# Performance work log

Hardware: AMD Instinct MI355X
Metric: run time of the kernel (lower is better)

## Reference

```python
import jax, jax.numpy as jnp
import numpy as np

S, H, NH, DS = 4096, 1024, 2, 64   # seq_len, hidden, num_heads, static_in_size
HD = H // NH                        # head_dim = 512
EPS = 1e-5                          # eqx.nn.LayerNorm default eps


def setup_inputs() -> dict:
    key = jax.random.key(0)
    ks = jax.random.split(key, 11)
    sc = lambda n: 1.0 / np.sqrt(n)
    return {
        "inputs": jax.random.normal(ks[0], (S, H), jnp.float32),
        "static_data": jax.random.normal(ks[1], (DS,), jnp.float32),
        "base_mask": jax.random.randint(ks[2], (S,), 0, 2).astype(bool),
        "Wq": jax.random.normal(ks[3], (H, H), jnp.float32) * sc(H),
        "Wk": jax.random.normal(ks[4], (H, H), jnp.float32) * sc(H),
        "Wv": jax.random.normal(ks[5], (H, H), jnp.float32) * sc(H),
        "Wo": jax.random.normal(ks[6], (H, H), jnp.float32) * sc(H),
        "Ws": jax.random.normal(ks[7], (H, DS), jnp.float32) * sc(DS),
        "bs": jax.random.normal(ks[8], (H,), jnp.float32) * 0.01,
        "ln_w": jnp.ones((H,), jnp.float32),
        "ln_b": jnp.zeros((H,), jnp.float32),
    }


def reference(inputs, static_data, base_mask, Wq, Wk, Wv, Wo, Ws, bs, ln_w, ln_b):
    # static embedding injected into keys/values
    semb = Ws @ static_data + bs                      # [H]
    kv_in = inputs + semb[None, :]                    # [S, H]

    # per-head projections (eqx Linear: y = W @ x, no bias in MHA projections)
    q = (inputs @ Wq.T).reshape(S, NH, HD)
    k = (kv_in @ Wk.T).reshape(S, NH, HD)
    v = (kv_in @ Wv.T).reshape(S, NH, HD)

    logits = jnp.einsum('qhd,khd->hqk', q, k) / np.sqrt(HD)  # [NH, S, S]

    # head 0: irregular mask (base_mask broadcast over queries); head 1: all-ones
    irregular = jnp.broadcast_to(base_mask[None, :], (S, S))
    mask = jnp.stack([irregular, jnp.ones((S, S), bool)], axis=0)  # [2, S, S]
    logits = jnp.where(mask, logits, jnp.finfo(logits.dtype).min)

    attn = jax.nn.softmax(logits, axis=-1)
    ctx = jnp.einsum('hqk,khd->qhd', attn, v).reshape(S, H)
    out = ctx @ Wo.T                                  # output projection

    # dropout_rate = 0 -> identity; residual + per-token LayerNorm
    res = out + inputs
    mu = res.mean(-1, keepdims=True)
    var = res.var(-1, keepdims=True)
    return (res - mu) / jnp.sqrt(var + EPS) * ln_w + ln_b
```

## Files before the change

### kernel.cpp

```cpp
#include <hip/hip_runtime.h>
#include <stdint.h>

#define S_LEN  4096
#define HID    1024
#define NHEAD  2
#define HDIM   512
#define KS_STRIDE 520
#define LN_EPS 1e-5f
#define PADK   4224
#define CH1    832

typedef __bf16 bf16x8 __attribute__((ext_vector_type(8)));
typedef float  f32x4  __attribute__((ext_vector_type(4)));

__device__ __forceinline__ float b2f(unsigned short u) {
    return __uint_as_float(((unsigned int)u) << 16);
}
__device__ __forceinline__ unsigned short f2b(float f) {
    unsigned int u = __float_as_uint(f);
    u += 0x7FFFu + ((u >> 16) & 1u);
    return (unsigned short)(u >> 16);
}

__device__ __forceinline__ void async_cp16(const void* g, void* l) {
    __builtin_amdgcn_global_load_lds(
        (const __attribute__((address_space(1))) unsigned int*)g,
        (__attribute__((address_space(3))) unsigned int*)l, 16, 0, 0);
}

__global__ void k_cvt4s(const float* __restrict__ i0, const float* __restrict__ i1,
                        const float* __restrict__ i2, const float* __restrict__ i3,
                        unsigned short* __restrict__ o0, unsigned short* __restrict__ o1,
                        unsigned short* __restrict__ o2, unsigned short* __restrict__ o3,
                        const float* __restrict__ Ws, const float* __restrict__ sd,
                        const float* __restrict__ bs, float* __restrict__ semb,
                        const int* __restrict__ msk, int* __restrict__ cidx,
                        int* __restrict__ nactp) {
    int z = blockIdx.y;
    if (z == 4) {
        int j = blockIdx.x * blockDim.x + threadIdx.x;
        if (j >= HID) return;
        float acc = bs[j];
        const float* row = Ws + j * 64;
        #pragma unroll
        for (int d = 0; d < 64; ++d) acc += row[d] * sd[d];
        semb[j] = acc;
        return;
    }
    if (z == 5) {
        if (blockIdx.x != 0) return;
        __shared__ int cnts[256];
        __shared__ int bases[256];
        __shared__ int nact_s;
        int t = threadIdx.x;
        int c = 0;
        #pragma unroll
        for (int i = 0; i < 16; ++i) c += (msk[t * 16 + i] != 0);
        cnts[t] = c;
        __syncthreads();
        if (t == 0) {
            int b = 0;
            for (int k = 0; k < 256; ++k) { bases[k] = b; b += cnts[k]; }
            nactp[0] = b;
            nact_s   = b;
        }
        __syncthreads();
        int b = bases[t];
        #pragma unroll
        for (int i = 0; i < 16; ++i)
            if (msk[t * 16 + i] != 0) cidx[b++] = t * 16 + i;
        for (int j = nact_s + t; j < PADK; j += 256) cidx[j] = 0;
        return;
    }
    const float* in = z == 0 ? i0 : z == 1 ? i1 : z == 2 ? i2 : i3;
    unsigned short* o = z == 0 ? o0 : z == 1 ? o1 : z == 2 ? o2 : o3;
    int i = (blockIdx.x * blockDim.x + threadIdx.x) * 8;
    float4 a = *(const float4*)(in + i);
    float4 b = *(const float4*)(in + i + 4);
    unsigned short r[8] = {f2b(a.x), f2b(a.y), f2b(a.z), f2b(a.w),
                           f2b(b.x), f2b(b.y), f2b(b.z), f2b(b.w)};
    *(uint4*)(o + i) = *(const uint4*)r;
}

__global__ void k_kvin(const float* __restrict__ X,
                       const float* __restrict__ semb,
                       unsigned short* __restrict__ Xb,
                       unsigned short* __restrict__ kv) {
    int idx = (blockIdx.x * blockDim.x + threadIdx.x) * 8;
    if (idx >= S_LEN * HID) return;
    int col = idx & (HID - 1);
    float4 a = *(const float4*)(X + idx);
    float4 b = *(const float4*)(X + idx + 4);
    unsigned short xo[8] = {f2b(a.x), f2b(a.y), f2b(a.z), f2b(a.w),
                            f2b(b.x), f2b(b.y), f2b(b.z), f2b(b.w)};
    *(uint4*)(Xb + idx) = *(const uint4*)xo;
    unsigned short o[8];
    o[0] = f2b(a.x + semb[col + 0]);
    o[1] = f2b(a.y + semb[col + 1]);
    o[2] = f2b(a.z + semb[col + 2]);
    o[3] = f2b(a.w + semb[col + 3]);
    o[4] = f2b(b.x + semb[col + 4]);
    o[5] = f2b(b.y + semb[col + 5]);
    o[6] = f2b(b.z + semb[col + 6]);
    o[7] = f2b(b.w + semb[col + 7]);
    *(uint4*)(kv + idx) = *(const uint4*)o;
}

__device__ __forceinline__
void gemm128(const unsigned short* __restrict__ A,
             const unsigned short* __restrict__ B,
             unsigned short* __restrict__ Cb,
             int bx, int nx, int ldc,
             const int* __restrict__ ra, const int* __restrict__ rb) {
    __shared__ unsigned short As[2][128 * 32];
    __shared__ unsigned short Bs[2][128 * 32];
    int tid  = threadIdx.x;
    int wave = tid >> 6, lane = tid & 63;
    int quad = lane >> 4, l16 = lane & 15;
    int wm = wave >> 1, wn = wave & 1;
    int m0 = (bx / nx) * 128, n0 = (bx % nx) * 128;

    auto stage = [&](int k0, int b) {
        #pragma unroll
        for (int i = 0; i < 2; ++i) {
            int c = tid + i * 256;
            int arow = m0 + (c >> 2);
            if (ra) arow = ra[arow];
            int brow = n0 + (c >> 2);
            if (rb) brow = rb[brow];
            async_cp16(A + (size_t)arow * HID + k0 + (c & 3) * 8, As[b] + c * 8);
            async_cp16(B + (size_t)brow * HID + k0 + (c & 3) * 8, Bs[b] + c * 8);
        }
    };

    f32x4 zero = {0.f, 0.f, 0.f, 0.f};
    f32x4 acc[4][4];
    #pragma unroll
    for (int i = 0; i < 4; ++i)
        #pragma unroll
        for (int j = 0; j < 4; ++j) acc[i][j] = zero;

    stage(0, 0);
    for (int it = 0; it < HID / 32; ++it) {
        int b = it & 1;
        __syncthreads();
        if (it + 1 < HID / 32) stage((it + 1) * 32, b ^ 1);

        bf16x8 af[4], bfr[4];
        #pragma unroll
        for (int i = 0; i < 4; ++i)
            af[i] = *(const bf16x8*)(As[b] + (wm * 64 + i * 16 + l16) * 32 + quad * 8);
        #pragma unroll
        for (int j = 0; j < 4; ++j)
            bfr[j] = *(const bf16x8*)(Bs[b] + (wn * 64 + j * 16 + l16) * 32 + quad * 8);
        #pragma unroll
        for (int i = 0; i < 4; ++i)
            #pragma unroll
            for (int j = 0; j < 4; ++j)
                acc[i][j] = __builtin_amdgcn_mfma_f32_16x16x32_bf16(af[i], bfr[j], acc[i][j], 0, 0, 0);
    }

    #pragma unroll
    for (int i = 0; i < 4; ++i) {
        int rbase = m0 + wm * 64 + i * 16 + quad * 4;
        #pragma unroll
        for (int j = 0; j < 4; ++j) {
            int col = n0 + wn * 64 + j * 16 + l16;
            #pragma unroll
            for (int r = 0; r < 4; ++r)
                Cb[(size_t)(rbase + r) * ldc + col] = f2b(acc[i][j][r]);
        }
    }
}

__global__ __launch_bounds__(256)
void k_gemms(const unsigned short* __restrict__ Xb,
             const unsigned short* __restrict__ kvin,
             const unsigned short* __restrict__ Wqb,
             const unsigned short* __restrict__ Wkb,
             const unsigned short* __restrict__ Wvb,
             const int* __restrict__ cidx,
             unsigned short* __restrict__ Qb,
             unsigned short* __restrict__ Kb1,
             unsigned short* __restrict__ Vt1,
             unsigned short* __restrict__ Kc,
             unsigned short* __restrict__ Vtc) {
    int g = blockIdx.x;
    int b = (g & 7) * 97 + (g >> 3);
    if (b < 256)      gemm128(Xb,   Wqb,             Qb,  b,        8, HID,   nullptr, nullptr);
    else if (b < 384) gemm128(kvin, Wkb + 512 * HID, Kb1, b - 256,  4, 512,   nullptr, nullptr);
    else if (b < 512) gemm128(Wvb + 512 * HID, kvin, Vt1, b - 384, 32, S_LEN, nullptr, nullptr);
    else if (b < 644) gemm128(kvin, Wkb,             Kc,  b - 512,  4, 512,   cidx,    nullptr);
    else              gemm128(Wvb,  kvin,            Vtc, b - 644, 33, PADK,  nullptr, cidx);
}

__global__ __launch_bounds__(256)
void k_gemm_o(const unsigned short* __restrict__ Opart,
              const float* __restrict__ Lbuf,
              const unsigned short* __restrict__ B,
              float* __restrict__ Cf,
              const float* __restrict__ Xres) {
    __shared__ unsigned short As[2][64 * 32];
    __shared__ unsigned short Bs[2][128 * 32];
    const size_t SH2 = (size_t)S_LEN * 512;
    int tid  = threadIdx.x;
    int wave = tid >> 6, lane = tid & 63;
    int quad = lane >> 4, l16 = lane & 15;
    int bx = (blockIdx.x & 7) * 64 + (blockIdx.x >> 3);
    int m0 = (bx >> 3) * 64, n0 = (bx & 7) * 128;

    int arow  = m0 + (tid >> 2);
    int acol8 = (tid & 3) * 8;
    float rinv[NHEAD];
    {
        float l0 = Lbuf[arow] + Lbuf[S_LEN + arow] + Lbuf[2 * S_LEN + arow];
        float l1 = 0.f;
        #pragma unroll
        for (int z = 3; z < 8; ++z) l1 += Lbuf[z * S_LEN + arow];
        rinv[0] = 1.f / l0;
        rinv[1] = 1.f / l1;
    }

    auto stageB = [&](int k0, int b) {
        #pragma unroll
        for (int i = 0; i < 2; ++i) {
            int c = tid + i * 256;
            async_cp16(B + (n0 + (c >> 2)) * HID + k0 + (c & 3) * 8, Bs[b] + c * 8);
        }
    };
    auto stageA = [&](int k0, int b) {
        int h = k0 >> 9;
        float rv = rinv[h];
        int lk = (k0 & 511) + acol8;
        const unsigned short* ap = Opart + (h ? 3 * SH2 : 0) + (size_t)arow * 512 + lk;
        float s[8] = {0.f, 0.f, 0.f, 0.f, 0.f, 0.f, 0.f, 0.f};
        int nz = h ? 5 : 3;
        for (int z = 0; z < nz; ++z) {
            uint4 v = *(const uint4*)(ap + (size_t)z * SH2);
            unsigned short us[8];
            *(uint4*)us = v;
            #pragma unroll
            for (int e = 0; e < 8; ++e) s[e] += b2f(us[e]);
        }
        unsigned short o8[8];
        #pragma unroll
        for (int e = 0; e < 8; ++e) o8[e] = f2b(s[e] * rv);
        *(uint4*)(As[b] + tid * 8) = *(const uint4*)o8;
    };

    f32x4 zero = {0.f, 0.f, 0.f, 0.f};
    f32x4 acc[4][2];
    #pragma unroll
    for (int i = 0; i < 4; ++i)
        #pragma unroll
        for (int j = 0; j < 2; ++j) acc[i][j] = zero;

    stageB(0, 0);
    stageA(0, 0);
    for (int it = 0; it < HID / 32; ++it) {
        int b = it & 1;
        __syncthreads();
        if (it + 1 < HID / 32) {
            stageB((it + 1) * 32, b ^ 1);
            stageA((it + 1) * 32, b ^ 1);
        }
        bf16x8 af[4], bfr[2];
        #pragma unroll
        for (int i = 0; i < 4; ++i)
            af[i] = *(const bf16x8*)(As[b] + (i * 16 + l16) * 32 + quad * 8);
        #pragma unroll
        for (int j = 0; j < 2; ++j)
            bfr[j] = *(const bf16x8*)(Bs[b] + (wave * 32 + j * 16 + l16) * 32 + quad * 8);
        #pragma unroll
        for (int i = 0; i < 4; ++i)
            #pragma unroll
            for (int j = 0; j < 2; ++j)
                acc[i][j] = __builtin_amdgcn_mfma_f32_16x16x32_bf16(af[i], bfr[j], acc[i][j], 0, 0, 0);
    }

    #pragma unroll
    for (int i = 0; i < 4; ++i) {
        int rbase = m0 + i * 16 + quad * 4;
        #pragma unroll
        for (int j = 0; j < 2; ++j) {
            int col = n0 + wave * 32 + j * 16 + l16;
            #pragma unroll
            for (int r = 0; r < 4; ++r) {
                size_t o = (size_t)(rbase + r) * HID + col;
                Cf[o] = acc[i][j][r] + Xres[o];
            }
        }
    }
}

__global__ __launch_bounds__(512, 2)
void k_flash(const unsigned short* __restrict__ Q,
             const unsigned short* __restrict__ Kb1,
             const unsigned short* __restrict__ Vt1,
             const unsigned short* __restrict__ Kc,
             const unsigned short* __restrict__ Vtc,
             const int* __restrict__ nactp,
             unsigned short* __restrict__ Opart,
             float* __restrict__ Lbuf) {
    __shared__ unsigned short Ks[2][32 * KS_STRIDE];
    __shared__ __bf16 Ps[2][128][40];
    int tid  = threadIdx.x;
    int wave = tid >> 6, lane = tid & 63;
    int quad = lane >> 4, l16 = lane & 15;
    int x = blockIdx.x, qtile = blockIdx.y;
    int head  = (x >= 3) ? 1 : 0;
    int split = head ? x - 3 : x;
    int nact  = nactp[0];

    int nit, base, vrs;
    const unsigned short *Ksrc, *Vsrc;
    if (head == 0) {
        nit  = (nact + 95) / 96;
        base = split * nit * 32;
        Ksrc = Kc;  Vsrc = Vtc; vrs = PADK;
    } else {
        base = split * CH1;
        nit  = min(CH1 >> 5, (S_LEN - base) >> 5);
        Ksrc = Kb1; Vsrc = Vt1; vrs = S_LEN;
    }

    int qrow = qtile * 128 + wave * 16 + l16;
    const unsigned short* qp = Q + qrow * HID + head * HDIM;
    bf16x8 qf[16];
    #pragma unroll
    for (int t = 0; t < 16; ++t) qf[t] = *(const bf16x8*)(qp + t * 32 + quad * 8);

    float lsum[4];
    #pragma unroll
    for (int r = 0; r < 4; ++r) lsum[r] = 0.f;
    f32x4 zero = {0.f, 0.f, 0.f, 0.f};
    f32x4 oacc[8][4];
    #pragma unroll
    for (int mt = 0; mt < 8; ++mt)
        #pragma unroll
        for (int nt = 0; nt < 4; ++nt) oacc[mt][nt] = zero;

    const float scale = 0.044194173824159216f;
    const unsigned short* vptr = Vsrc + (size_t)(wave * 64 + l16) * vrs + base + quad * 8;

    auto stageK = [&](int kt, int buf) {
        int kb = base + kt * 32;
        #pragma unroll
        for (int i = 0; i < 4; ++i) {
            int c = tid + i * 512;
            int row = c >> 6, col = (c & 63) * 8;
            async_cp16(Ksrc + (size_t)(kb + row) * 512 + col, &Ks[buf][row * KS_STRIDE + col]);
        }
    };

    if (nit > 0) stageK(0, 0);

    bf16x8 vf[4];
    for (int it = 0; it < nit; ++it) {
        int cur = it & 1;
        __syncthreads();

        if (it + 1 < nit) stageK(it + 1, cur ^ 1);

        __builtin_amdgcn_s_setprio(1);
        if (it > 0) {
            #pragma unroll
            for (int mt = 0; mt < 8; ++mt) {
                bf16x8 pf = *(const bf16x8*)&Ps[cur ^ 1][mt * 16 + l16][quad * 8];
                #pragma unroll
                for (int nt = 0; nt < 4; ++nt)
                    oacc[mt][nt] = __builtin_amdgcn_mfma_f32_16x16x32_bf16(pf, vf[nt], oacc[mt][nt], 0, 0, 0);
            }
        }

        #pragma unroll
        for (int nt = 0; nt < 4; ++nt)
            vf[nt] = *(const bf16x8*)(vptr + (size_t)nt * 16 * vrs + it * 32);

        f32x4 sacc[2];
        sacc[0] = zero; sacc[1] = zero;
        #pragma unroll
        for (int nt = 0; nt < 2; ++nt)
            #pragma unroll
            for (int t = 0; t < 16; ++t) {
                bf16x8 kf = *(const bf16x8*)&Ks[cur][(nt * 16 + l16) * KS_STRIDE + t * 32 + quad * 8];
                sacc[nt] = __builtin_amdgcn_mfma_f32_16x16x32_bf16(qf[t], kf, sacc[nt], 0, 0, 0);
            }
        __builtin_amdgcn_s_setprio(0);

        bool keep0 = true, keep1 = true;
        if (head == 0) {
            int kb = base + it * 32;
            keep0 = kb + l16 < nact;
            keep1 = kb + 16 + l16 < nact;
        }
        #pragma unroll
        for (int r = 0; r < 4; ++r) {
            float p0 = keep0 ? __expf(fminf(sacc[0][r] * scale, 30.f)) : 0.f;
            float p1 = keep1 ? __expf(fminf(sacc[1][r] * scale, 30.f)) : 0.f;
            lsum[r] += p0 + p1;
            Ps[cur][wave * 16 + quad * 4 + r][l16]      = (__bf16)p0;
            Ps[cur][wave * 16 + quad * 4 + r][16 + l16] = (__bf16)p1;
        }
    }

    if (nit > 0) {
        int lastb = (nit - 1) & 1;
        __syncthreads();
        #pragma unroll
        for (int mt = 0; mt < 8; ++mt) {
            bf16x8 pf = *(const bf16x8*)&Ps[lastb][mt * 16 + l16][quad * 8];
            #pragma unroll
            for (int nt = 0; nt < 4; ++nt)
                oacc[mt][nt] = __builtin_amdgcn_mfma_f32_16x16x32_bf16(pf, vf[nt], oacc[mt][nt], 0, 0, 0);
        }
    }

    #pragma unroll
    for (int r = 0; r < 4; ++r) {
        float s = lsum[r];
        #pragma unroll
        for (int off = 1; off < 16; off <<= 1)
            s += __shfl_xor(s, off, 64);
        lsum[r] = s;
    }
    int slot = head ? 3 + split : split;
    int lrow = qtile * 128 + wave * 16 + quad * 4;
    if (l16 == 0) {
        #pragma unroll
        for (int r = 0; r < 4; ++r)
            Lbuf[slot * S_LEN + lrow + r] = lsum[r];
    }
    unsigned short* op = Opart + (size_t)slot * S_LEN * 512;
    #pragma unroll
    for (int mt = 0; mt < 8; ++mt)
        #pragma unroll
        for (int nt = 0; nt < 4; ++nt)
            #pragma unroll
            for (int r = 0; r < 4; ++r)
                op[(qtile * 128 + mt * 16 + quad * 4 + r) * 512 +
                   wave * 64 + nt * 16 + l16] = f2b(oacc[mt][nt][r]);
}

__global__ __launch_bounds__(256)
void k_ln(const float* __restrict__ res,
          const float* __restrict__ w,
          const float* __restrict__ b,
          float* __restrict__ out) {
    __shared__ float red[8];
    int s = blockIdx.x, tid = threadIdx.x;
    const float* row = res + s * HID;
    float x[4], s1 = 0.f, s2 = 0.f;
    #pragma unroll
    for (int i = 0; i < 4; ++i) {
        x[i] = row[tid + i * 256];
        s1 += x[i]; s2 += x[i] * x[i];
    }
    #pragma unroll
    for (int off = 1; off < 64; off <<= 1) {
        s1 += __shfl_xor(s1, off, 64);
        s2 += __shfl_xor(s2, off, 64);
    }
    int wave = tid >> 6;
    if ((tid & 63) == 0) { red[wave] = s1; red[4 + wave] = s2; }
    __syncthreads();
    s1 = red[0] + red[1] + red[2] + red[3];
    s2 = red[4] + red[5] + red[6] + red[7];
    float mu   = s1 * (1.f / HID);
    float var  = s2 * (1.f / HID) - mu * mu;
    float rstd = rsqrtf(var + LN_EPS);
    #pragma unroll
    for (int i = 0; i < 4; ++i) {
        int col = tid + i * 256;
        out[s * HID + col] = (x[i] - mu) * rstd * w[col] + b[col];
    }
}

extern "C" void kernel_launch(void* const* d_in, const int* in_sizes, int n_in,
                              void* d_out, int out_size, void* d_ws, size_t ws_size,
                              hipStream_t stream) {
    const float* X   = (const float*)d_in[0];
    const float* sd  = (const float*)d_in[1];
    const int*   msk = (const int*)d_in[2];
    const float* Wq  = (const float*)d_in[3];
    const float* Wk  = (const float*)d_in[4];
    const float* Wv  = (const float*)d_in[5];
    const float* Wo  = (const float*)d_in[6];
    const float* Wsp = (const float*)d_in[7];
    const float* bsp = (const float*)d_in[8];
    const float* lw  = (const float*)d_in[9];
    const float* lb  = (const float*)d_in[10];
    float* out = (float*)d_out;

    char* ws = (char*)d_ws;
    const size_t MB = 1ull << 20;
    float*          semb  = (float*)(ws);
    int*            cidx  = (int*)(ws + (16 << 10));
    int*            nactp = (int*)(ws + (48 << 10));
    float*          Lbuf  = (float*)(ws + (1ull << 16));
    unsigned short* Xb    = (unsigned short*)(ws + 1 * MB);
    unsigned short* kvin  = (unsigned short*)(ws + 9 * MB);
    unsigned short* Qb    = (unsigned short*)(ws + 17 * MB);
    unsigned short* Kb1   = (unsigned short*)(ws + 25 * MB);
    unsigned short* Vt1   = (unsigned short*)(ws + 29 * MB);
    unsigned short* Kc    = (unsigned short*)(ws + 33 * MB);
    unsigned short* Vtc   = (unsigned short*)(ws + 37 * MB + (256 << 10));
    unsigned short* Wqb   = (unsigned short*)(ws + 49 * MB);
    unsigned short* Wkb   = (unsigned short*)(ws + 51 * MB);
    unsigned short* Wvb   = (unsigned short*)(ws + 53 * MB);
    unsigned short* Wob   = (unsigned short*)(ws + 55 * MB);
    float*          resf  = (float*)(ws + 17 * MB);
    unsigned short* Opart = (unsigned short*)(ws + 57 * MB);

    const int SH = S_LEN * HID;
    const int WW = HID * HID;

    k_cvt4s<<<dim3(WW / 8 / 256, 6), dim3(256), 0, stream>>>(
        Wq, Wk, Wv, Wo, Wqb, Wkb, Wvb, Wob, Wsp, sd, bsp, semb, msk, cidx, nactp);

    k_kvin<<<dim3(SH / 8 / 256), dim3(256), 0, stream>>>(X, semb, Xb, kvin);

    k_gemms<<<dim3(776), dim3(256), 0, stream>>>(
        Xb, kvin, Wqb, Wkb, Wvb, cidx, Qb, Kb1, Vt1, Kc, Vtc);

    k_flash<<<dim3(8, S_LEN / 128), dim3(512), 0, stream>>>(
        Qb, Kb1, Vt1, Kc, Vtc, nactp, Opart, Lbuf);

    k_gemm_o<<<dim3(512), dim3(256), 0, stream>>>(Opart, Lbuf, Wob, resf, X);
    k_ln<<<dim3(S_LEN), dim3(256), 0, stream>>>(resf, lw, lb, out);
}
```

Before: 269.0 us.

## Fold static embedding into K/V GEMM bias, merge prep kernels, skip inactive tiles

```diff
diff --git a/kernel.cpp b/kernel.cpp
--- a/kernel.cpp
+++ b/kernel.cpp
@@ -35,11 +35,23 @@
                         const float* __restrict__ Ws, const float* __restrict__ sd,
                         const float* __restrict__ bs, float* __restrict__ semb,
                         const int* __restrict__ msk, int* __restrict__ cidx,
-                        int* __restrict__ nactp) {
-    int z = blockIdx.y;
-    if (z == 4) {
-        int j = blockIdx.x * blockDim.x + threadIdx.x;
-        if (j >= HID) return;
+                        int* __restrict__ nactp,
+                        const float* __restrict__ X, unsigned short* __restrict__ Xb) {
+    int b = blockIdx.x, tid = threadIdx.x;
+    if (b < 2048) {
+        int w = b >> 9, inner = b & 511;
+        const float* in = w == 0 ? i0 : w == 1 ? i1 : w == 2 ? i2 : i3;
+        unsigned short* o = w == 0 ? o0 : w == 1 ? o1 : w == 2 ? o2 : o3;
+        int i = (inner * 256 + tid) * 8;
+        float4 a = *(const float4*)(in + i);
+        float4 c = *(const float4*)(in + i + 4);
+        unsigned short r[8] = {f2b(a.x), f2b(a.y), f2b(a.z), f2b(a.w),
+                               f2b(c.x), f2b(c.y), f2b(c.z), f2b(c.w)};
+        *(uint4*)(o + i) = *(const uint4*)r;
+        return;
+    }
+    if (b < 2052) {
+        int j = (b - 2048) * 256 + tid;
         float acc = bs[j];
         const float* row = Ws + j * 64;
         #pragma unroll
@@ -47,63 +59,38 @@
         semb[j] = acc;
         return;
     }
-    if (z == 5) {
-        if (blockIdx.x != 0) return;
+    if (b == 2052) {
         __shared__ int cnts[256];
         __shared__ int bases[256];
         __shared__ int nact_s;
-        int t = threadIdx.x;
+        int t = tid;
         int c = 0;
         #pragma unroll
         for (int i = 0; i < 16; ++i) c += (msk[t * 16 + i] != 0);
         cnts[t] = c;
         __syncthreads();
         if (t == 0) {
-            int b = 0;
-            for (int k = 0; k < 256; ++k) { bases[k] = b; b += cnts[k]; }
-            nactp[0] = b;
-            nact_s   = b;
+            int bb = 0;
+            for (int k = 0; k < 256; ++k) { bases[k] = bb; bb += cnts[k]; }
+            nactp[0] = bb;
+            nact_s   = bb;
         }
         __syncthreads();
-        int b = bases[t];
+        int bb = bases[t];
         #pragma unroll
         for (int i = 0; i < 16; ++i)
-            if (msk[t * 16 + i] != 0) cidx[b++] = t * 16 + i;
+            if (msk[t * 16 + i] != 0) cidx[bb++] = t * 16 + i;
         for (int j = nact_s + t; j < PADK; j += 256) cidx[j] = 0;
         return;
     }
-    const float* in = z == 0 ? i0 : z == 1 ? i1 : z == 2 ? i2 : i3;
-    unsigned short* o = z == 0 ? o0 : z == 1 ? o1 : z == 2 ? o2 : o3;
-    int i = (blockIdx.x * blockDim.x + threadIdx.x) * 8;
-    float4 a = *(const float4*)(in + i);
-    float4 b = *(const float4*)(in + i + 4);
-    unsigned short r[8] = {f2b(a.x), f2b(a.y), f2b(a.z), f2b(a.w),
-                           f2b(b.x), f2b(b.y), f2b(b.z), f2b(b.w)};
-    *(uint4*)(o + i) = *(const uint4*)r;
-}
-
-__global__ void k_kvin(const float* __restrict__ X,
-                       const float* __restrict__ semb,
-                       unsigned short* __restrict__ Xb,
-                       unsigned short* __restrict__ kv) {
-    int idx = (blockIdx.x * blockDim.x + threadIdx.x) * 8;
-    if (idx >= S_LEN * HID) return;
-    int col = idx & (HID - 1);
-    float4 a = *(const float4*)(X + idx);
-    float4 b = *(const float4*)(X + idx + 4);
-    unsigned short xo[8] = {f2b(a.x), f2b(a.y), f2b(a.z), f2b(a.w),
-                            f2b(b.x), f2b(b.y), f2b(b.z), f2b(b.w)};
-    *(uint4*)(Xb + idx) = *(const uint4*)xo;
-    unsigned short o[8];
-    o[0] = f2b(a.x + semb[col + 0]);
-    o[1] = f2b(a.y + semb[col + 1]);
-    o[2] = f2b(a.z + semb[col + 2]);
-    o[3] = f2b(a.w + semb[col + 3]);
-    o[4] = f2b(b.x + semb[col + 4]);
-    o[5] = f2b(b.y + semb[col + 5]);
-    o[6] = f2b(b.z + semb[col + 6]);
-    o[7] = f2b(b.w + semb[col + 7]);
-    *(uint4*)(kv + idx) = *(const uint4*)o;
+    {
+        int idx = ((b - 2053) * 256 + tid) * 8;
+        float4 a = *(const float4*)(X + idx);
+        float4 c = *(const float4*)(X + idx + 4);
+        unsigned short r[8] = {f2b(a.x), f2b(a.y), f2b(a.z), f2b(a.w),
+                               f2b(c.x), f2b(c.y), f2b(c.z), f2b(c.w)};
+        *(uint4*)(Xb + idx) = *(const uint4*)r;
+    }
 }
 
 __device__ __forceinline__
@@ -111,14 +98,30 @@
              const unsigned short* __restrict__ B,
              unsigned short* __restrict__ Cb,
              int bx, int nx, int ldc,
-             const int* __restrict__ ra, const int* __restrict__ rb) {
+             const int* __restrict__ ra, const int* __restrict__ rb,
+             const float* __restrict__ semb, int bmode) {
     __shared__ unsigned short As[2][128 * 32];
     __shared__ unsigned short Bs[2][128 * 32];
+    __shared__ float pb[256];
     int tid  = threadIdx.x;
     int wave = tid >> 6, lane = tid & 63;
     int quad = lane >> 4, l16 = lane & 15;
     int wm = wave >> 1, wn = wave & 1;
     int m0 = (bx / nx) * 128, n0 = (bx % nx) * 128;
+
+    if (bmode) {
+        const unsigned short* wb = (bmode == 1 ? B : A)
+            + (size_t)((bmode == 1 ? n0 : m0) + (tid >> 1)) * HID + (tid & 1) * 512;
+        const float* se = semb + (tid & 1) * 512;
+        float s = 0.f;
+        #pragma unroll 8
+        for (int d = 0; d < 512; d += 8) {
+            bf16x8 w8 = *(const bf16x8*)(wb + d);
+            #pragma unroll
+            for (int e = 0; e < 8; ++e) s += (float)w8[e] * se[d + e];
+        }
+        pb[tid] = s;
+    }
 
     auto stage = [&](int k0, int b) {
         #pragma unroll
@@ -166,20 +169,32 @@
         #pragma unroll
         for (int j = 0; j < 4; ++j) {
             int col = n0 + wn * 64 + j * 16 + l16;
-            #pragma unroll
-            for (int r = 0; r < 4; ++r)
-                Cb[(size_t)(rbase + r) * ldc + col] = f2b(acc[i][j][r]);
+            float bvc = 0.f;
+            if (bmode == 1) {
+                int cl = wn * 64 + j * 16 + l16;
+                bvc = pb[2 * cl] + pb[2 * cl + 1];
+            }
+            #pragma unroll
+            for (int r = 0; r < 4; ++r) {
+                float v = acc[i][j][r] + bvc;
+                if (bmode == 2) {
+                    int rl = wm * 64 + i * 16 + quad * 4 + r;
+                    v += pb[2 * rl] + pb[2 * rl + 1];
+                }
+                Cb[(size_t)(rbase + r) * ldc + col] = f2b(v);
+            }
         }
     }
 }
 
 __global__ __launch_bounds__(256)
 void k_gemms(const unsigned short* __restrict__ Xb,
-             const unsigned short* __restrict__ kvin,
              const unsigned short* __restrict__ Wqb,
              const unsigned short* __restrict__ Wkb,
              const unsigned short* __restrict__ Wvb,
              const int* __restrict__ cidx,
+             const int* __restrict__ nactp,
+             const float* __restrict__ semb,
              unsigned short* __restrict__ Qb,
              unsigned short* __restrict__ Kb1,
              unsigned short* __restrict__ Vt1,
@@ -187,11 +202,23 @@
              unsigned short* __restrict__ Vtc) {
     int g = blockIdx.x;
     int b = (g & 7) * 97 + (g >> 3);
-    if (b < 256)      gemm128(Xb,   Wqb,             Qb,  b,        8, HID,   nullptr, nullptr);
-    else if (b < 384) gemm128(kvin, Wkb + 512 * HID, Kb1, b - 256,  4, 512,   nullptr, nullptr);
-    else if (b < 512) gemm128(Wvb + 512 * HID, kvin, Vt1, b - 384, 32, S_LEN, nullptr, nullptr);
-    else if (b < 644) gemm128(kvin, Wkb,             Kc,  b - 512,  4, 512,   cidx,    nullptr);
-    else              gemm128(Wvb,  kvin,            Vtc, b - 644, 33, PADK,  nullptr, cidx);
+    if (b < 256) {
+        gemm128(Xb, Wqb, Qb, b, 8, HID, nullptr, nullptr, semb, 0);
+    } else if (b < 384) {
+        gemm128(Xb, Wkb + 512 * HID, Kb1, b - 256, 4, 512, nullptr, nullptr, semb, 1);
+    } else if (b < 512) {
+        gemm128(Wvb + 512 * HID, Xb, Vt1, b - 384, 32, S_LEN, nullptr, nullptr, semb, 2);
+    } else if (b < 644) {
+        int bb = b - 512;
+        int kcLim = ((nactp[0] + 95) / 96) * 96;
+        if ((bb >> 2) * 128 >= kcLim) return;
+        gemm128(Xb, Wkb, Kc, bb, 4, 512, cidx, nullptr, semb, 1);
+    } else {
+        int bb = b - 644;
+        int kcLim = ((nactp[0] + 95) / 96) * 96;
+        if ((bb % 33) * 128 >= kcLim) return;
+        gemm128(Wvb, Xb, Vtc, bb, 33, PADK, nullptr, cidx, semb, 2);
+    }
 }
 
 __global__ __launch_bounds__(256)
@@ -499,7 +526,6 @@
     int*            nactp = (int*)(ws + (48 << 10));
     float*          Lbuf  = (float*)(ws + (1ull << 16));
     unsigned short* Xb    = (unsigned short*)(ws + 1 * MB);
-    unsigned short* kvin  = (unsigned short*)(ws + 9 * MB);
     unsigned short* Qb    = (unsigned short*)(ws + 17 * MB);
     unsigned short* Kb1   = (unsigned short*)(ws + 25 * MB);
     unsigned short* Vt1   = (unsigned short*)(ws + 29 * MB);
@@ -512,16 +538,11 @@
     float*          resf  = (float*)(ws + 17 * MB);
     unsigned short* Opart = (unsigned short*)(ws + 57 * MB);
 
-    const int SH = S_LEN * HID;
-    const int WW = HID * HID;
-
-    k_cvt4s<<<dim3(WW / 8 / 256, 6), dim3(256), 0, stream>>>(
-        Wq, Wk, Wv, Wo, Wqb, Wkb, Wvb, Wob, Wsp, sd, bsp, semb, msk, cidx, nactp);
-
-    k_kvin<<<dim3(SH / 8 / 256), dim3(256), 0, stream>>>(X, semb, Xb, kvin);
+    k_cvt4s<<<dim3(4101), dim3(256), 0, stream>>>(
+        Wq, Wk, Wv, Wo, Wqb, Wkb, Wvb, Wob, Wsp, sd, bsp, semb, msk, cidx, nactp, X, Xb);
 
     k_gemms<<<dim3(776), dim3(256), 0, stream>>>(
-        Xb, kvin, Wqb, Wkb, Wvb, cidx, Qb, Kb1, Vt1, Kc, Vtc);
+        Xb, Wqb, Wkb, Wvb, cidx, nactp, semb, Qb, Kb1, Vt1, Kc, Vtc);
 
     k_flash<<<dim3(8, S_LEN / 128), dim3(512), 0, stream>>>(
         Qb, Kb1, Vt1, Kc, Vtc, nactp, Opart, Lbuf);
```

Result: slower. 327.3 us (+21.7%).
